# Kernel tuning notes

Hardware: AMD Instinct MI355X
Metric: run time of the kernel (lower is better)

## Reference

```python
import jax, jax.numpy as jnp
import numpy as np

GCN_DEPTH = 2
PROP_ALPHA = 0.05
TANH_ALPHA = 3.0
SUBGRAPH = 20
SCALE_SET = (1.0, 0.8, 0.6, 0.5)
LAYERS = 3


def _tconv(x, W, b, stride):
    # x: (B,C,N,L), W: (O,I,1,k) -> VALID temporal conv along L
    y = jax.lax.conv_general_dilated(x, W, (1, stride), 'VALID',
                                     dimension_numbers=('NCHW', 'OIHW', 'NCHW'))
    return y + b[None, :, None, None]


def _build_adj(feat_scale, emb1, emb2, W1, b1, W2, b2, sfac):
    # dynamic graph: time-pooled scale features + static node embeddings
    feat = feat_scale.mean(axis=3).transpose(0, 2, 1)            # (B,N,C)
    n1 = jnp.tanh(TANH_ALPHA * sfac * (feat @ W1 + b1 + emb1))   # (B,N,D)
    n2 = jnp.tanh(TANH_ALPHA * sfac * (feat @ W2 + b2 + emb2))
    a = jnp.einsum('bnd,bmd->bnm', n1, n2) - jnp.einsum('bnd,bmd->bnm', n2, n1)
    adj = jax.nn.relu(jnp.tanh(TANH_ALPHA * a))                  # (B,N,N)
    kth = jax.lax.top_k(adj, SUBGRAPH)[0][..., -1:]              # per-row k-th value
    return adj * (adj >= kth).astype(adj.dtype)


def _mixprop(x, adj, W, b):
    # x: (B,C,N,L), adj: (B,N,N); gcn_depth-step alpha-mixed diffusion
    N = x.shape[2]
    A = adj + jnp.eye(N, dtype=adj.dtype)
    A = A / A.sum(axis=2, keepdims=True)
    h = x
    out = [h]
    for _ in range(GCN_DEPTH):
        h = PROP_ALPHA * x + (1.0 - PROP_ALPHA) * jnp.einsum('bcvl,bvw->bcwl', h, A)
        out.append(h)
    ho = jnp.concatenate(out, axis=1)                            # (B,(gdep+1)C,N,L)
    return jnp.einsum('bcnl,co->bonl', ho, W) + b[None, :, None, None]


def _forward(x, Ws, bs, scW0, scW1, scW2, scb, emb1, emb2,
             lin1W, lin1b, lin2W, lin2b, gW, gb,
             svW0, svW1, svW2, svb, s0W, s0b,
             gfW1, gfW2, e1W, e1b, e2W, e2b):
    # multi-scale block: 1x1 start conv then strided temporal convs
    h = jnp.einsum('bcnl,oc->bonl', x, Ws) + bs[None, :, None, None]
    scW = [scW0, scW1, scW2]
    scales = []
    for i in range(LAYERS):
        h = _tconv(h, scW[i], scb[i], 1 if i == 0 else 2)
        scales.append(h)
    # per-scale dynamic adjacency
    adjs = [_build_adj(scales[i], emb1, emb2, lin1W[i], lin1b[i],
                       lin2W[i], lin2b[i], SCALE_SET[i]) for i in range(LAYERS)]
    # scale0 head over raw input (dropout is identity in eval mode)
    out0 = jnp.einsum('bcnl,ocl->bon', x, s0W)[..., None] + s0b[None, :, None, None]
    outs = [out0]
    svW = [svW0, svW1, svW2]
    for i in range(LAYERS):
        g = (_mixprop(scales[i], adjs[i], gW[i, 0], gb[i, 0])
             + _mixprop(scales[i], adjs[i].transpose(0, 2, 1), gW[i, 1], gb[i, 1]))
        outs.append(jnp.einsum('bcnl,ocl->bon', g, svW[i])[..., None]
                    + svb[i][None, :, None, None])
    cat = jnp.concatenate(outs, axis=1)          # (B,(L+1)*Cs,N,1)
    stk = jnp.stack(outs, axis=1)                # (B,L+1,Cs,N,1)
    # SE-style gated fusion over scales
    se = cat.mean(axis=2)[..., 0]                # (B,(L+1)*Cs)
    se = jax.nn.sigmoid(jax.nn.relu(se @ gfW1) @ gfW2)   # (B,L+1)
    fused = (stk * se[:, :, None, None, None]).mean(axis=1)  # (B,Cs,N,1)
    y = jax.nn.relu(fused)
    y = jax.nn.relu(jnp.einsum('bcnl,oc->bonl', y, e1W) + e1b[None, :, None, None])
    y = jnp.einsum('bcnl,oc->bonl', y, e2W) + e2b[None, :, None, None]
    return y, jnp.stack(adjs)


def setup_inputs() -> dict:
    key = jax.random.key(0)
    ks = jax.random.split(key, 27)
    B, N, S, D = 4, 600, 168, 40
    Cc, Cs, Ce, Od = 32, 16, 128, 12
    L = [162, 79, 39]
    K = [7, 6, 3]
    r = lambda k, sh, s=0.1: jax.random.normal(k, sh, jnp.float32) * s
    return {
        'x': jax.random.normal(ks[0], (B, 1, N, S), jnp.float32),
        'Ws': r(ks[1], (Cc, 1)), 'bs': r(ks[2], (Cc,)),
        'scW0': r(ks[3], (Cc, Cc, 1, K[0])), 'scW1': r(ks[4], (Cc, Cc, 1, K[1])),
        'scW2': r(ks[5], (Cc, Cc, 1, K[2])), 'scb': r(ks[6], (3, Cc)),
        'emb1': r(ks[7], (N, D), 1.0), 'emb2': r(ks[8], (N, D), 1.0),
        'lin1W': r(ks[9], (3, Cc, D)), 'lin1b': r(ks[10], (3, D)),
        'lin2W': r(ks[11], (3, Cc, D)), 'lin2b': r(ks[12], (3, D)),
        'gW': r(ks[13], (3, 2, 3 * Cc, Cc)), 'gb': r(ks[14], (3, 2, Cc)),
        'svW0': r(ks[15], (Cs, Cc, L[0])), 'svW1': r(ks[16], (Cs, Cc, L[1])),
        'svW2': r(ks[17], (Cs, Cc, L[2])), 'svb': r(ks[18], (3, Cs)),
        's0W': r(ks[19], (Cs, 1, S)), 's0b': r(ks[20], (Cs,)),
        'gfW1': r(ks[21], (4 * Cs, 4)), 'gfW2': r(ks[22], (4, 4)),
        'e1W': r(ks[23], (Ce, Cs)), 'e1b': r(ks[24], (Ce,)),
        'e2W': r(ks[25], (Od, Ce)), 'e2b': r(ks[26], (Od,)),
    }


def reference(x, Ws, bs, scW0, scW1, scW2, scb, emb1, emb2,
              lin1W, lin1b, lin2W, lin2b, gW, gb,
              svW0, svW1, svW2, svb, s0W, s0b,
              gfW1, gfW2, e1W, e1b, e2W, e2b):
    return _forward(x, Ws, bs, scW0, scW1, scW2, scb, emb1, emb2,
                    lin1W, lin1b, lin2W, lin2b, gW, gb,
                    svW0, svW1, svW2, svb, s0W, s0b,
                    gfW1, gfW2, e1W, e1b, e2W, e2b)
```

## Files before the change

### kernel.cpp

```cpp
#include <hip/hip_runtime.h>
#include <math.h>


#define DW_WEFF 0
#define DW_CC   1536
#define FB      3264
#define OW_CSV  (FB+0)
#define OW_CBIG (FB+48)
#define OW_VBIG (FB+304)
#define OW_U    (FB+43312)
#define OW_T    (FB+760112)
#define OW_FEAT (FB+1374512)
#define OW_N1   (FB+1604912)
#define OW_N2   (FB+1892912)
#define OW_IRA  (FB+2180912)
#define OW_IRB  (FB+2188112)
#define OW_U1A  (FB+2195312)
#define OW_U2A  (FB+2310512)
#define OW_U1B  (FB+2425712)
#define OW_U2B  (FB+2540912)
#define OW_U3A  (FB+2656112)
#define OW_U3B  (FB+2771312)
#define OW_O    (FB+2886512)
#define OW_SE   (FB+3040112)

__device__ const int UOFF_[3] = {0, 414720, 616960};

__device__ __forceinline__ float tanh_eigen(float x)
{
  const float CL = 7.99881172180175781f;
  float xc = fminf(fmaxf(x, -CL), CL);
  float x2 = __fmul_rn(xc, xc);
  float p = fmaf(x2, -2.76076847742355e-16f, 2.00018790482477e-13f);
  p = fmaf(x2, p, -8.60467152213735e-11f);
  p = fmaf(x2, p, 5.12229709037114e-08f);
  p = fmaf(x2, p, 1.48572235717979e-05f);
  p = fmaf(x2, p, 6.37261928875436e-04f);
  p = fmaf(x2, p, 4.89352455891786e-03f);
  p = __fmul_rn(xc, p);
  float q = fmaf(x2, 1.19825839466702e-06f, 1.18534705686654e-04f);
  q = fmaf(x2, q, 2.26843463243900e-03f);
  q = fmaf(x2, q, 4.89352518554385e-03f);
  float r = __fdiv_rn(p, q);
  return fabsf(x) < 0.0004f ? x : r;
}

__global__ __launch_bounds__(256) void k_pre_wc(const float* Ws, const float* bs,
    const float* scW0, const float* scW1, const float* scW2, const float* scb,
    const float* svW0, const float* svW1, const float* svW2,
    const float* gb, const float* svb, double* wd, float* ws)
{
  if (blockIdx.x < 48) {
    int blk = blockIdx.x;
    int i = blk/16, o = blk%16;
    const float* svW = (i==0)?svW0:((i==1)?svW1:svW2);
    int L = (i==0)?162:((i==1)?79:39);
    int tid = threadIdx.x;
    __shared__ double red[256];
    double s = 0;
    for (int idx = tid; idx < 32*L; idx += 256) {
      int o2 = idx / L, l = idx - o2*L;
      s += (double)svW[(o*32+o2)*L + l] * ((double)gb[(i*2+0)*32+o2] + (double)gb[(i*2+1)*32+o2]);
    }
    red[tid] = s; __syncthreads();
    for (int st = 128; st; st >>= 1) { if (tid < st) red[tid] += red[tid+st]; __syncthreads(); }
    if (tid == 0) ws[OW_CSV + blk] = (float)(red[0] + (double)svb[i*16+o]);
    return;
  }
  __shared__ double w0[32][7], c0[32], w1[32][12], c1[32];
  int t = threadIdx.x;
  for (int e = t; e < 32*7; e += 256) {
    int c = e/7, p = e%7; double s = 0;
    for (int ci = 0; ci < 32; ci++) s += (double)scW0[(c*32+ci)*7+p] * (double)Ws[ci];
    w0[c][p] = s;
  }
  for (int e = t; e < 32; e += 256) {
    double s = 0;
    for (int ci = 0; ci < 32; ci++) { double a = 0; for (int p = 0; p < 7; p++) a += (double)scW0[(e*32+ci)*7+p]; s += a*(double)bs[ci]; }
    c0[e] = s + (double)scb[e];
  }
  __syncthreads();
  for (int e = t; e < 32*12; e += 256) {
    int c = e/12, m = e%12; double s = 0;
    for (int k1 = 0; k1 < 6; k1++) { int k0 = m - k1; if (k0 < 0 || k0 > 6) continue;
      for (int ci = 0; ci < 32; ci++) s += (double)scW1[(c*32+ci)*6+k1] * w0[ci][k0]; }
    w1[c][m] = s;
  }
  for (int e = t; e < 32; e += 256) {
    double s = 0;
    for (int ci = 0; ci < 32; ci++) { double a = 0; for (int k1 = 0; k1 < 6; k1++) a += (double)scW1[(e*32+ci)*6+k1]; s += a*c0[ci]; }
    c1[e] = s + (double)scb[32+e];
  }
  __syncthreads();
  for (int e = t; e < 32*16; e += 256) {
    int c = e/16, p = e%16; double s = 0;
    for (int k2 = 0; k2 < 3; k2++) { int m = p - 2*k2; if (m < 0 || m > 11) continue;
      for (int ci = 0; ci < 32; ci++) s += (double)scW2[(c*32+ci)*3+k2] * w1[ci][m]; }
    wd[DW_WEFF + (2*32+c)*16 + p] = s;
  }
  for (int e = t; e < 32; e += 256) {
    double s = 0;
    for (int ci = 0; ci < 32; ci++) { double a = 0; for (int k2 = 0; k2 < 3; k2++) a += (double)scW2[(e*32+ci)*3+k2]; s += a*c1[ci]; }
    wd[DW_CC + 64 + e] = s + (double)scb[64+e];
  }
  for (int e = t; e < 32*7;  e += 256) wd[DW_WEFF + (e/7)*16  + e%7 ] = w0[e/7][e%7];
  for (int e = t; e < 32*12; e += 256) wd[DW_WEFF + (32 + e/12)*16 + e%12] = w1[e/12][e%12];
  for (int e = t; e < 32; e += 256) { wd[DW_CC+e] = c0[e]; wd[DW_CC+32+e] = c1[e]; }
}

__global__ void k_pre_u(const float* svW0, const float* svW1, const float* svW2,
                        const float* gW, float* ws)
{
  int blk = blockIdx.x;
  int i, L, base; const float* svW;
  if (blk < 1620)      { i=0; L=162; svW=svW0; base=0; }
  else if (blk < 2410) { i=1; L=79;  svW=svW1; base=1620; }
  else                 { i=2; L=39;  svW=svW2; base=2410; }
  int e = (blk-base)*256 + threadIdx.x;
  int total = 5*16*32*L;
  if (e >= total) return;
  int l = e % L, c = (e/L) % 32, o = (e/(L*32)) % 16, g = e/(L*32*16);
  const float* gW0 = gW + (i*2+0)*96*32;
  const float* gW1 = gW + (i*2+1)*96*32;
  float s = 0.f;
  for (int o2 = 0; o2 < 32; o2++) {
    float w;
    if (g == 0) w = gW0[c*32+o2] + gW1[c*32+o2]
                  + 0.05f*(gW0[(32+c)*32+o2] + gW0[(64+c)*32+o2] + gW1[(32+c)*32+o2] + gW1[(64+c)*32+o2]);
    else if (g == 1) w = gW0[(32+c)*32+o2];
    else if (g == 2) w = gW0[(64+c)*32+o2];
    else if (g == 3) w = gW1[(32+c)*32+o2];
    else             w = gW1[(64+c)*32+o2];
    s += svW[(o*32+o2)*L + l] * w;
  }
  ws[OW_U + UOFF_[i] + ((g*16+o)*32 + c)*L + l] = s;
}

__global__ __launch_bounds__(256) void k_pre_v(const float* s0W, const float* s0b, double* wd, float* ws)
{
  int jj = blockIdx.x;
  int tid = threadIdx.x;
  if (jj >= 240) {
    int o = jj - 240;
    if (tid < 168) ws[OW_VBIG + jj*168 + tid] = s0W[o*168 + tid];
    if (tid == 0)  ws[OW_CBIG + jj] = s0b[o];
    return;
  }
  int i = jj/80, g = (jj%80)/16, o = jj%16;
  int st = (i==0)?1:((i==1)?2:4), tp = (i==0)?7:((i==1)?12:16), L = (i==0)?162:((i==1)?79:39);
  const float* Ui = ws + OW_U + UOFF_[i] + ((g*16+o)*32)*L;
  __shared__ float uls[32*162];
  __shared__ double weff_s[32*16];
  __shared__ double cc_s[32];
  __shared__ double red[256];
  int NL = 32*L;
  for (int e = tid; e < NL; e += 256) uls[e] = Ui[e];
  for (int e = tid; e < 32*16; e += 256) weff_s[e] = wd[DW_WEFF + (i*32)*16 + e];
  if (tid < 32) cc_s[tid] = wd[DW_CC + i*32 + tid];
  __syncthreads();
  double s = 0;
  for (int e = tid; e < NL; e += 256) s += (double)uls[e] * cc_s[e / L];
  red[tid] = s; __syncthreads();
  for (int stp = 128; stp; stp >>= 1) { if (tid < stp) red[tid] += red[tid+stp]; __syncthreads(); }
  if (tid == 0) ws[OW_CBIG + jj] = (float)red[0];
  if (tid < 168) {
    int u = tid;
    int lo_ = u - tp + 1;
    int lmin = lo_ > 0 ? (lo_ + st - 1)/st : 0;
    int lmax = u/st; if (lmax > L-1) lmax = L-1;
    double v = 0.0;
    for (int c = 0; c < 32; c++) {
      const float* uc = uls + c*L;
      const double* wc = weff_s + c*16;
      for (int l = lmin; l <= lmax; l++)
        v += (double)uc[l] * wc[u - st*l];
    }
    ws[OW_VBIG + jj*168 + u] = (float)v;
  }
}

__global__ __launch_bounds__(256) void k_fg(const float* x, double* wd, float* ws)
{
  int t = threadIdx.x;
  if (blockIdx.x >= 300) {
    __shared__ float xs[16][168];
    int r0 = (blockIdx.x - 300)*16;
    for (int e = t; e < 16*168; e += 256) { int r = e/168, u = e%168; xs[r][u] = x[(r0+r)*168 + u]; }
    __syncthreads();
    int jj = t;
    const float* V = ws + OW_VBIG + jj*168;
    double a[16];
    #pragma unroll
    for (int r = 0; r < 16; r++) a[r] = 0;
    for (int u = 0; u < 168; u++) {
      float wv = V[u];
      #pragma unroll
      for (int r = 0; r < 16; r++) a[r] += (double)wv * (double)xs[r][u];
    }
    double cb = (double)ws[OW_CBIG + jj];
    for (int r = 0; r < 16; r++)
      ws[OW_T + (r0+r)*256 + jj] = (float)(a[r] + cb);
    return;
  }
  int blk = blockIdx.x;
  int b = blk / 75, n0 = (blk % 75) * 8;
  __shared__ float xsf[8][168];
  __shared__ double xbar[8][35];
  for (int e = t; e < 8*168; e += 256) xsf[e/168][e%168] = x[(b*600 + n0 + e/168)*168 + e%168];
  __syncthreads();
  for (int e = t; e < 8*35; e += 256) {
    int nn = e/35, slot = e%35;
    int i = slot < 7 ? 0 : (slot < 19 ? 1 : 2);
    int p = slot - (i==0?0:(i==1?7:19));
    int st = (i==0)?1:((i==1)?2:4), L = (i==0)?162:((i==1)?79:39);
    double s = 0;
    for (int l = 0; l < L; l++) s += (double)xsf[nn][st*l+p];
    xbar[nn][slot] = s / (double)L;
  }
  __syncthreads();
  int nn = t >> 5, c = t & 31;
  for (int i = 0; i < 3; i++) {
    int off = (i==0)?0:((i==1)?7:19), tp = (i==0)?7:((i==1)?12:16);
    double f = wd[DW_CC + i*32 + c];
    for (int p = 0; p < tp; p++) f += wd[DW_WEFF + (i*32+c)*16 + p] * xbar[nn][off+p];
    ws[OW_FEAT + ((i*4+b)*600 + n0+nn)*32 + c] = (float)f;
  }
}

__global__ __launch_bounds__(256) void k_nodes(const float* lin1W, const float* lin1b,
                                               const float* lin2W, const float* lin2b,
                                               const float* emb1, const float* emb2, float* ws)
{
  int blk = blockIdx.x;
  int nt = blk % 38, b = (blk/38) % 4, i = blk/152;
  int n0 = nt*16;
  __shared__ float W1[1280], W2[1280], b1[40], b2[40], sf[16][33];
  int t = threadIdx.x;
  for (int e = t; e < 1280; e += 256) { W1[e] = lin1W[i*1280 + e]; W2[e] = lin2W[i*1280 + e]; }
  if (t < 40) { b1[t] = lin1b[i*40 + t]; b2[t] = lin2b[i*40 + t]; }
  for (int e = t; e < 16*32; e += 256) {
    int nn = e >> 5, c = e & 31; int n = n0 + nn;
    sf[nn][c] = (n < 600) ? ws[OW_FEAT + ((i*4+b)*600 + n)*32 + c] : 0.f;
  }
  __syncthreads();
  const float TSF[3] = {3.0f, 2.4f, 1.8f};
  for (int item = t; item < 16*80; item += 256) {
    int nn = item / 80, rr = item % 80;
    int n = n0 + nn; if (n >= 600) continue;
    int which = rr/40, d = rr%40;
    const float* W  = which ? W2 : W1;
    const float* bv = which ? b2 : b1;
    const float* em = which ? emb2 : emb1;
    float pre = 0.f;
    #pragma unroll
    for (int c = 0; c < 32; c++) pre = fmaf(sf[nn][c], W[c*40+d], pre);
    float p2 = __fadd_rn(pre, bv[d]);
    float p3 = __fadd_rn(p2, em[n*40+d]);
    float arg = __fmul_rn(TSF[i], p3);
    ws[(which ? OW_N2 : OW_N1) + ((i*4+b)*600 + n)*40 + d] = tanh_eigen(arg);
  }
}

__device__ __forceinline__ float4 adj_ld(const float* n1, const float* n2, int e, int w0)
{
  int mat = e >= 320; int idx = e - 320*mat;
  int jj = idx/10, q = idx - 10*jj;
  int w = w0 + jj;
  if (w < 600) return *(const float4*)((mat ? n2 : n1) + w*40 + 4*q);
  float4 z; z.x = z.y = z.z = z.w = 0.f; return z;
}

__global__ __launch_bounds__(256) void k_adj(float* adj_out, float* ws)
{
  int blk = blockIdx.x;
  int tile = blk % 75, b = (blk/75) % 4, i = blk/300;
  int row0 = tile*8;
  const float* n1 = ws + OW_N1 + (i*4+b)*24000;
  const float* n2 = ws + OW_N2 + (i*4+b)*24000;
  __shared__ float c1s[32][44], c2s[32][44];
  __shared__ float svals[8][604];
  int t = threadIdx.x;
  int rc = t & 7, jc = t >> 3;
  float am1[40], am2[40];
  {
    const float4* m1p = (const float4*)(n1 + (row0 + rc)*40);
    const float4* m2p = (const float4*)(n2 + (row0 + rc)*40);
    #pragma unroll
    for (int q = 0; q < 10; q++) {
      float4 v1 = m1p[q], v2 = m2p[q];
      am1[4*q]=v1.x; am1[4*q+1]=v1.y; am1[4*q+2]=v1.z; am1[4*q+3]=v1.w;
      am2[4*q]=v2.x; am2[4*q+1]=v2.y; am2[4*q+2]=v2.z; am2[4*q+3]=v2.w;
    }
  }
  float4 s0 = adj_ld(n1, n2, t, 0);
  float4 s1 = adj_ld(n1, n2, t + 256, 0);
  float4 s2; if (t < 128) s2 = adj_ld(n1, n2, t + 512, 0);
  for (int k = 0; k < 19; k++) {
    int w0 = 32*k;
    __syncthreads();
    {
      int e = t;       { int mat=e>=320, idx=e-320*mat, jj=idx/10, q=idx-10*jj, w=w0+jj;
                         if (w<600) *(float4*)(&(mat?c2s:c1s)[jj][4*q]) = s0; }
      e = t + 256;     { int mat=e>=320, idx=e-320*mat, jj=idx/10, q=idx-10*jj, w=w0+jj;
                         if (w<600) *(float4*)(&(mat?c2s:c1s)[jj][4*q]) = s1; }
      if (t < 128) { e = t + 512; int mat=e>=320, idx=e-320*mat, jj=idx/10, q=idx-10*jj, w=w0+jj;
                         if (w<600) *(float4*)(&(mat?c2s:c1s)[jj][4*q]) = s2; }
    }
    __syncthreads();
    if (k < 18) {
      int w0n = w0 + 32;
      s0 = adj_ld(n1, n2, t, w0n);
      s1 = adj_ld(n1, n2, t + 256, w0n);
      if (t < 128) s2 = adj_ld(n1, n2, t + 512, w0n);
    }
    int w = w0 + jc;
    if (w < 600) {
      const float4* c2p = (const float4*)c2s[jc];
      const float4* c1p = (const float4*)c1s[jc];
      float d1 = 0.f, d2 = 0.f;
      #pragma unroll
      for (int q = 0; q < 10; q++) {
        float4 v = c2p[q];
        d1 = fmaf(am1[4*q], v.x, d1); d1 = fmaf(am1[4*q+1], v.y, d1);
        d1 = fmaf(am1[4*q+2], v.z, d1); d1 = fmaf(am1[4*q+3], v.w, d1);
      }
      #pragma unroll
      for (int q = 0; q < 10; q++) {
        float4 v = c1p[q];
        d2 = fmaf(am2[4*q], v.x, d2); d2 = fmaf(am2[4*q+1], v.y, d2);
        d2 = fmaf(am2[4*q+2], v.z, d2); d2 = fmaf(am2[4*q+3], v.w, d2);
      }
      float af = __fsub_rn(d1, d2);
      float tv = __fmul_rn(3.0f, af);
      float v = tanh_eigen(tv);
      svals[rc][w] = v > 0.f ? v : 0.f;
    }
  }
  __syncthreads();
  int r = t >> 5, j = t & 31;
  float vv[19];
  #pragma unroll
  for (int k = 0; k < 19; k++) {
    int w = j + 32*k;
    vv[k] = (w < 600) ? svals[r][w] : 0.f;
  }
  float rm = 0.f;
  #pragma unroll
  for (int k = 0; k < 19; k++) rm = fmaxf(rm, vv[k]);
  #pragma unroll
  for (int s = 16; s; s >>= 1) rm = fmaxf(rm, __shfl_xor(rm, s, 32));
  const float VP = tanh_eigen(8.0f);
  unsigned int vpb = __float_as_uint(VP);
  int cntp = 0;
  #pragma unroll
  for (int k = 0; k < 19; k++) { int w = j + 32*k; if (w < 600 && __float_as_uint(vv[k]) >= vpb) cntp++; }
  #pragma unroll
  for (int s = 16; s; s >>= 1) cntp += __shfl_xor(cntp, s, 32);
  unsigned int lo, hi;
  unsigned int mb1 = __float_as_uint(rm) + 1u;
  if (cntp >= 20) { lo = vpb; hi = mb1; }
  else            { lo = 0u;  hi = vpb < mb1 ? vpb : mb1; }
  while (hi - lo > 1u) {
    unsigned int mid = lo + ((hi - lo) >> 1);
    int cnt = 0;
    #pragma unroll
    for (int k = 0; k < 19; k++) {
      int w = j + 32*k;
      if (w < 600 && __float_as_uint(vv[k]) >= mid) cnt++;
    }
    #pragma unroll
    for (int s = 16; s; s >>= 1) cnt += __shfl_xor(cnt, s, 32);
    if (cnt >= 20) lo = mid; else hi = mid;
  }
  unsigned int kb = lo;
  float* arow = adj_out + (i*4+b)*360000 + (row0+r)*600;
  float rsum = 0.f;
  #pragma unroll
  for (int k = 0; k < 19; k++) {
    int w = j + 32*k;
    if (w < 600) {
      float v = (__float_as_uint(vv[k]) >= kb) ? vv[k] : 0.f;
      arow[w] = v;
      rsum += v;
    }
  }
  #pragma unroll
  for (int s = 16; s; s >>= 1) rsum += __shfl_xor(rsum, s, 32);
  if (j == 0) ws[OW_IRA + (i*4+b)*600 + row0 + r] = 1.f/(1.f + rsum);
}

__global__ __launch_bounds__(256) void k_invrb(const float* adj, float* ws)
{
  int blk = blockIdx.x;
  int ib = blk / 10, wt = blk % 10;
  int tid = threadIdx.x;
  int wl = tid & 63, vg = tid >> 6;
  int w = wt*64 + wl;
  const float* A = adj + ib*360000;
  float s = 0.f;
  if (w < 600) {
    for (int v = vg*150; v < vg*150 + 150; v++) s += A[v*600 + w];
  }
  __shared__ float red[4][64];
  red[vg][wl] = s;
  __syncthreads();
  if (vg == 0 && w < 600) {
    float tot = ((red[0][wl] + red[1][wl]) + red[2][wl]) + red[3][wl];
    ws[OW_IRB + ib*600 + w] = 1.f/(1.f + tot);
  }
}

__global__ __launch_bounds__(256) void k_prop1(const float* adj, float* ws)
{
  int blk = blockIdx.x;
  int wt = blk % 19;
  int d  = (blk / 19) & 1;
  int ib = blk / 38;
  int i = ib >> 2, b = ib & 3;
  int w0 = wt * 32;
  const float* A   = adj + ib*360000;
  const float* irx = ws + (d ? OW_IRB : OW_IRA) + ib*600;
  const float* Tb  = ws + OW_T + (b*600)*256 + i*80 + 16 + d*32;
  __shared__ float As[4][32][36];
  __shared__ float Zs[4][32][36];
  __shared__ float red[3][64][17];
  int tid = threadIdx.x;
  int wv = tid >> 6, ln = tid & 63;
  int wq = ln >> 3, oq = ln & 7;
  float acc[4][4];
  #pragma unroll
  for (int a1 = 0; a1 < 4; a1++)
    #pragma unroll
    for (int a2 = 0; a2 < 4; a2++) acc[a1][a2] = 0.f;
  int vbeg = wv*160, vend = vbeg + 160 < 600 ? vbeg + 160 : 600;
  for (int v0 = vbeg; v0 < vend; v0 += 32) {
    if (d == 0) {
      #pragma unroll
      for (int q = 0; q < 4; q++) {
        int m = q*64 + ln, rr = m >> 3, c4 = (m & 7)*4;
        int v = v0 + rr;
        float4 av; av.x = av.y = av.z = av.w = 0.f;
        if (v < 600) {
          int wb = w0 + c4;
          if (wb + 3 < 600) av = *(const float4*)(A + v*600 + wb);
          else {
            if (wb+0 < 600) av.x = A[v*600 + wb+0];
            if (wb+1 < 600) av.y = A[v*600 + wb+1];
            if (wb+2 < 600) av.z = A[v*600 + wb+2];
            if (wb+3 < 600) av.w = A[v*600 + wb+3];
          }
        }
        *(float4*)(&As[wv][rr][c4]) = av;
      }
    } else {
      #pragma unroll
      for (int q = 0; q < 4; q++) {
        int m = q*64 + ln, rr = m >> 3, c4 = (m & 7)*4;
        int w = w0 + rr;
        float4 av; av.x = av.y = av.z = av.w = 0.f;
        if (w < 600) {
          if (v0 + c4 + 3 < 600) av = *(const float4*)(A + w*600 + v0 + c4);
          else {
            if (v0+c4+0 < 600) av.x = A[w*600 + v0+c4+0];
            if (v0+c4+1 < 600) av.y = A[w*600 + v0+c4+1];
            if (v0+c4+2 < 600) av.z = A[w*600 + v0+c4+2];
            if (v0+c4+3 < 600) av.w = A[w*600 + v0+c4+3];
          }
        }
        As[wv][c4+0][rr] = av.x; As[wv][c4+1][rr] = av.y;
        As[wv][c4+2][rr] = av.z; As[wv][c4+3][rr] = av.w;
      }
    }
    #pragma unroll
    for (int q = 0; q < 4; q++) {
      int m = q*64 + ln, rr = m >> 3, c4 = (m & 7)*4;
      int v = v0 + rr;
      float4 zv; zv.x = zv.y = zv.z = zv.w = 0.f;
      if (v < 600) {
        float ir = irx[v];
        float4 tv = *(const float4*)(Tb + v*256 + c4);
        zv.x = ir*tv.x; zv.y = ir*tv.y; zv.z = ir*tv.z; zv.w = ir*tv.w;
      }
      *(float4*)(&Zs[wv][rr][c4]) = zv;
    }
    __builtin_amdgcn_s_waitcnt(0);
    for (int vl = 0; vl < 32; vl++) {
      float4 a4 = *(const float4*)(&As[wv][vl][wq*4]);
      float4 z4 = *(const float4*)(&Zs[wv][vl][oq*4]);
      acc[0][0] = fmaf(a4.x, z4.x, acc[0][0]); acc[0][1] = fmaf(a4.x, z4.y, acc[0][1]);
      acc[0][2] = fmaf(a4.x, z4.z, acc[0][2]); acc[0][3] = fmaf(a4.x, z4.w, acc[0][3]);
      acc[1][0] = fmaf(a4.y, z4.x, acc[1][0]); acc[1][1] = fmaf(a4.y, z4.y, acc[1][1]);
      acc[1][2] = fmaf(a4.y, z4.z, acc[1][2]); acc[1][3] = fmaf(a4.y, z4.w, acc[1][3]);
      acc[2][0] = fmaf(a4.z, z4.x, acc[2][0]); acc[2][1] = fmaf(a4.z, z4.y, acc[2][1]);
      acc[2][2] = fmaf(a4.z, z4.z, acc[2][2]); acc[2][3] = fmaf(a4.z, z4.w, acc[2][3]);
      acc[3][0] = fmaf(a4.w, z4.x, acc[3][0]); acc[3][1] = fmaf(a4.w, z4.y, acc[3][1]);
      acc[3][2] = fmaf(a4.w, z4.z, acc[3][2]); acc[3][3] = fmaf(a4.w, z4.w, acc[3][3]);
    }
  }
  if (wv > 0) {
    #pragma unroll
    for (int kw = 0; kw < 4; kw++)
      #pragma unroll
      for (int ko = 0; ko < 4; ko++) red[wv-1][ln][kw*4+ko] = acc[kw][ko];
  }
  __syncthreads();
  if (wv == 0) {
    #pragma unroll
    for (int kw = 0; kw < 4; kw++) {
      int w = w0 + wq*4 + kw;
      if (w >= 600) continue;
      float irw = irx[w];
      #pragma unroll
      for (int ko = 0; ko < 4; ko++) {
        int oz = oq*4 + ko;
        float sum = acc[kw][ko] + red[0][ln][kw*4+ko] + red[1][ln][kw*4+ko] + red[2][ln][kw*4+ko];
        sum += irw * Tb[w*256 + oz];
        float* dst = ws + (d==0 ? (oz < 16 ? OW_U1A : OW_U2A) : (oz < 16 ? OW_U1B : OW_U2B));
        dst[(ib*600 + w)*16 + (oz & 15)] = sum;
      }
    }
  }
}

__global__ __launch_bounds__(256) void k_prop2(const float* adj, float* ws)
{
  int blk = blockIdx.x;
  int wt = blk % 19;
  int d  = (blk / 19) & 1;
  int ib = blk / 38;
  int w0 = wt * 32;
  const float* A   = adj + ib*360000;
  const float* irx = ws + (d ? OW_IRB : OW_IRA) + ib*600;
  const float* u2x = ws + (d ? OW_U2B : OW_U2A) + ib*9600;
  __shared__ float As[4][32][36];
  __shared__ float Zs[4][32][20];
  __shared__ float red[3][64][9];
  int tid = threadIdx.x;
  int wv = tid >> 6, ln = tid & 63;
  int wq = ln >> 3, oq = ln & 7;
  float acc[4][2];
  #pragma unroll
  for (int a1 = 0; a1 < 4; a1++) { acc[a1][0] = 0.f; acc[a1][1] = 0.f; }
  int vbeg = wv*160, vend = vbeg + 160 < 600 ? vbeg + 160 : 600;
  for (int v0 = vbeg; v0 < vend; v0 += 32) {
    if (d == 0) {
      #pragma unroll
      for (int q = 0; q < 4; q++) {
        int m = q*64 + ln, rr = m >> 3, c4 = (m & 7)*4;
        int v = v0 + rr;
        float4 av; av.x = av.y = av.z = av.w = 0.f;
        if (v < 600) {
          int wb = w0 + c4;
          if (wb + 3 < 600) av = *(const float4*)(A + v*600 + wb);
          else {
            if (wb+0 < 600) av.x = A[v*600 + wb+0];
            if (wb+1 < 600) av.y = A[v*600 + wb+1];
            if (wb+2 < 600) av.z = A[v*600 + wb+2];
            if (wb+3 < 600) av.w = A[v*600 + wb+3];
          }
        }
        *(float4*)(&As[wv][rr][c4]) = av;
      }
    } else {
      #pragma unroll
      for (int q = 0; q < 4; q++) {
        int m = q*64 + ln, rr = m >> 3, c4 = (m & 7)*4;
        int w = w0 + rr;
        float4 av; av.x = av.y = av.z = av.w = 0.f;
        if (w < 600) {
          if (v0 + c4 + 3 < 600) av = *(const float4*)(A + w*600 + v0 + c4);
          else {
            if (v0+c4+0 < 600) av.x = A[w*600 + v0+c4+0];
            if (v0+c4+1 < 600) av.y = A[w*600 + v0+c4+1];
            if (v0+c4+2 < 600) av.z = A[w*600 + v0+c4+2];
            if (v0+c4+3 < 600) av.w = A[w*600 + v0+c4+3];
          }
        }
        As[wv][c4+0][rr] = av.x; As[wv][c4+1][rr] = av.y;
        As[wv][c4+2][rr] = av.z; As[wv][c4+3][rr] = av.w;
      }
    }
    #pragma unroll
    for (int q = 0; q < 2; q++) {
      int m = q*64 + ln, rr = m >> 2, c4 = (m & 3)*4;
      int v = v0 + rr;
      float4 zv; zv.x = zv.y = zv.z = zv.w = 0.f;
      if (v < 600) {
        float ir = irx[v];
        float4 uv = *(const float4*)(u2x + v*16 + c4);
        zv.x = ir*uv.x; zv.y = ir*uv.y; zv.z = ir*uv.z; zv.w = ir*uv.w;
      }
      *(float4*)(&Zs[wv][rr][c4]) = zv;
    }
    __builtin_amdgcn_s_waitcnt(0);
    for (int vl = 0; vl < 32; vl++) {
      float4 a4 = *(const float4*)(&As[wv][vl][wq*4]);
      float2 z2 = *(const float2*)(&Zs[wv][vl][oq*2]);
      acc[0][0] = fmaf(a4.x, z2.x, acc[0][0]); acc[0][1] = fmaf(a4.x, z2.y, acc[0][1]);
      acc[1][0] = fmaf(a4.y, z2.x, acc[1][0]); acc[1][1] = fmaf(a4.y, z2.y, acc[1][1]);
      acc[2][0] = fmaf(a4.z, z2.x, acc[2][0]); acc[2][1] = fmaf(a4.z, z2.y, acc[2][1]);
      acc[3][0] = fmaf(a4.w, z2.x, acc[3][0]); acc[3][1] = fmaf(a4.w, z2.y, acc[3][1]);
    }
  }
  if (wv > 0) {
    #pragma unroll
    for (int kw = 0; kw < 4; kw++) {
      red[wv-1][ln][kw*2+0] = acc[kw][0];
      red[wv-1][ln][kw*2+1] = acc[kw][1];
    }
  }
  __syncthreads();
  if (wv == 0) {
    float* dst = ws + (d==0 ? OW_U3A : OW_U3B);
    #pragma unroll
    for (int kw = 0; kw < 4; kw++) {
      int w = w0 + wq*4 + kw;
      if (w >= 600) continue;
      float irw = irx[w];
      #pragma unroll
      for (int ko = 0; ko < 2; ko++) {
        int oz = oq*2 + ko;
        float sum = acc[kw][ko] + red[0][ln][kw*2+ko] + red[1][ln][kw*2+ko] + red[2][ln][kw*2+ko];
        sum += irw * u2x[w*16 + oz];
        dst[(ib*600 + w)*16 + oz] = sum;
      }
    }
  }
}

__global__ void k_outs(float* ws)
{
  int e = blockIdx.x*256 + threadIdx.x;
  if (e >= 153600) return;
  int n = e % 600, o = (e/600) % 16, b = (e/9600) % 4, s = e/38400;
  float val;
  if (s == 0) {
    val = ws[OW_T + (b*600+n)*256 + 240 + o];
  } else {
    int i = s - 1;
    int idx = ((i*4+b)*600 + n)*16 + o;
    float t0 = ws[OW_T + (b*600+n)*256 + i*80 + o];
    val = t0 + 0.95f  * (ws[OW_U1A+idx] + ws[OW_U1B+idx])
             + 0.0475f* (ws[OW_U2A+idx] + ws[OW_U2B+idx])
             + 0.9025f* (ws[OW_U3A+idx] + ws[OW_U3B+idx])
             + ws[OW_CSV + i*16 + o];
  }
  ws[OW_O + ((s*4+b)*16 + o)*600 + n] = val;
}

__global__ void k_se(const float* gfW1, const float* gfW2, float* ws)
{
  __shared__ float sv[4][64], hb[4][4];
  int t = threadIdx.x, b = t >> 6, k = t & 63;
  const float* Op = ws + OW_O + (((k>>4)*4 + b)*16 + (k & 15))*600;
  float s = 0.f;
  for (int n = 0; n < 600; n++) s += Op[n];
  sv[b][k] = s * (1.f/600.f);
  __syncthreads();
  if (t < 16) {
    int bb = t >> 2, j = t & 3;
    float h = 0.f;
    for (int kk = 0; kk < 64; kk++) h += sv[bb][kk]*gfW1[kk*4+j];
    hb[bb][j] = h > 0.f ? h : 0.f;
  }
  __syncthreads();
  if (t < 16) {
    int bb = t >> 2, ii = t & 3;
    float g = 0.f;
    for (int j = 0; j < 4; j++) g += hb[bb][j]*gfW2[j*4+ii];
    ws[OW_SE + bb*4 + ii] = 1.f/(1.f + expf(-g));
  }
}

__global__ __launch_bounds__(128) void k_head(const float* e1W, const float* e1b,
                                              const float* e2W, const float* e2b,
                                              float* ws, float* dout)
{
  int blk = blockIdx.x, b = blk/600, n = blk%600;
  __shared__ float y0[16], y1[128];
  int t = threadIdx.x;
  if (t < 16) {
    float f = 0.f;
    for (int s = 0; s < 4; s++) f += ws[OW_SE + b*4 + s] * ws[OW_O + ((s*4+b)*16 + t)*600 + n];
    f *= 0.25f;
    y0[t] = f > 0.f ? f : 0.f;
  }
  __syncthreads();
  {
    float h = e1b[t];
    for (int o = 0; o < 16; o++) h += e1W[t*16+o]*y0[o];
    y1[t] = h > 0.f ? h : 0.f;
  }
  __syncthreads();
  if (t < 96) {
    int o = t >> 3, part = t & 7;
    float v = 0.f;
    #pragma unroll
    for (int e = 0; e < 16; e++) v = fmaf(e2W[o*128 + part*16 + e], y1[part*16 + e], v);
    #pragma unroll
    for (int s = 4; s; s >>= 1) v += __shfl_down(v, s, 8);
    if (part == 0) dout[b*7200 + o*600 + n] = e2b[o] + v;
  }
}

extern "C" void kernel_launch(void* const* d_in, const int* in_sizes, int n_in,
                              void* d_out, int out_size, void* d_ws, size_t ws_size,
                              hipStream_t stream)
{
  const float* x    = (const float*)d_in[0];
  const float* Ws   = (const float*)d_in[1];
  const float* bs   = (const float*)d_in[2];
  const float* scW0 = (const float*)d_in[3];
  const float* scW1 = (const float*)d_in[4];
  const float* scW2 = (const float*)d_in[5];
  const float* scb  = (const float*)d_in[6];
  const float* emb1 = (const float*)d_in[7];
  const float* emb2 = (const float*)d_in[8];
  const float* lin1W= (const float*)d_in[9];
  const float* lin1b= (const float*)d_in[10];
  const float* lin2W= (const float*)d_in[11];
  const float* lin2b= (const float*)d_in[12];
  const float* gW   = (const float*)d_in[13];
  const float* gb   = (const float*)d_in[14];
  const float* svW0 = (const float*)d_in[15];
  const float* svW1 = (const float*)d_in[16];
  const float* svW2 = (const float*)d_in[17];
  const float* svb  = (const float*)d_in[18];
  const float* s0W  = (const float*)d_in[19];
  const float* s0b  = (const float*)d_in[20];
  const float* gfW1 = (const float*)d_in[21];
  const float* gfW2 = (const float*)d_in[22];
  const float* e1W  = (const float*)d_in[23];
  const float* e1b  = (const float*)d_in[24];
  const float* e2W  = (const float*)d_in[25];
  const float* e2b  = (const float*)d_in[26];
  float* out = (float*)d_out;
  float* ws  = (float*)d_ws;
  double* wd = (double*)d_ws;
  float* adj_out = out + 28800;

  k_pre_wc<<<49, 256, 0, stream>>>(Ws, bs, scW0, scW1, scW2, scb,
                                   svW0, svW1, svW2, gb, svb, wd, ws);
  k_pre_u<<<2800, 256, 0, stream>>>(svW0, svW1, svW2, gW, ws);
  k_pre_v<<<256, 256, 0, stream>>>(s0W, s0b, wd, ws);
  k_fg<<<450, 256, 0, stream>>>(x, wd, ws);
  k_nodes<<<456, 256, 0, stream>>>(lin1W, lin1b, lin2W, lin2b, emb1, emb2, ws);
  k_adj<<<900, 256, 0, stream>>>(adj_out, ws);
  k_invrb<<<120, 256, 0, stream>>>(adj_out, ws);
  k_prop1<<<456, 256, 0, stream>>>(adj_out, ws);
  k_prop2<<<456, 256, 0, stream>>>(adj_out, ws);
  k_outs<<<600, 256, 0, stream>>>(ws);
  k_se<<<1, 256, 0, stream>>>(gfW1, gfW2, ws);
  k_head<<<2400, 128, 0, stream>>>(e1W, e1b, e2W, e2b, ws, out);
}
```

Before: 266.5 us.

## Merge weight-precompute kernels and read adjacency node vectors directly from global

Folds the k_pre_u blocks into k_pre_wc as extra blocks of a single launch, removing one kernel launch and its inter-kernel gap. In k_adj, the double-buffered shared-memory staging of n1/n2 column tiles and its two per-iteration barriers are replaced by direct float4 loads from global memory, relying on cache for reuse. This cuts barriers and shared-memory traffic but may add global/L2 load pressure, since the 8 threads sharing a column each fetch it themselves.

```diff
diff --git a/kernel.cpp b/kernel.cpp
--- a/kernel.cpp
+++ b/kernel.cpp
@@ -45,26 +45,52 @@
   return fabsf(x) < 0.0004f ? x : r;
 }
 
-__global__ __launch_bounds__(256) void k_pre_wc(const float* Ws, const float* bs,
+__global__ __launch_bounds__(256) void k_pre_wcu(const float* Ws, const float* bs,
     const float* scW0, const float* scW1, const float* scW2, const float* scb,
     const float* svW0, const float* svW1, const float* svW2,
-    const float* gb, const float* svb, double* wd, float* ws)
-{
+    const float* gb, const float* svb, const float* gW, double* wd, float* ws)
+{
+  if (blockIdx.x >= 49) {
+    int blk = blockIdx.x - 49;
+    int i, L, base; const float* svW;
+    if (blk < 1620)      { i=0; L=162; svW=svW0; base=0; }
+    else if (blk < 2410) { i=1; L=79;  svW=svW1; base=1620; }
+    else                 { i=2; L=39;  svW=svW2; base=2410; }
+    int e = (blk-base)*256 + threadIdx.x;
+    int total = 5*16*32*L;
+    if (e >= total) return;
+    int l = e % L, c = (e/L) % 32, o = (e/(L*32)) % 16, g = e/(L*32*16);
+    const float* gW0 = gW + (i*2+0)*96*32;
+    const float* gW1 = gW + (i*2+1)*96*32;
+    float s = 0.f;
+    for (int o2 = 0; o2 < 32; o2++) {
+      float w;
+      if (g == 0) w = gW0[c*32+o2] + gW1[c*32+o2]
+                    + 0.05f*(gW0[(32+c)*32+o2] + gW0[(64+c)*32+o2] + gW1[(32+c)*32+o2] + gW1[(64+c)*32+o2]);
+      else if (g == 1) w = gW0[(32+c)*32+o2];
+      else if (g == 2) w = gW0[(64+c)*32+o2];
+      else if (g == 3) w = gW1[(32+c)*32+o2];
+      else             w = gW1[(64+c)*32+o2];
+      s += svW[(o*32+o2)*L + l] * w;
+    }
+    ws[OW_U + UOFF_[i] + ((g*16+o)*32 + c)*L + l] = s;
+    return;
+  }
   if (blockIdx.x < 48) {
     int blk = blockIdx.x;
     int i = blk/16, o = blk%16;
     const float* svW = (i==0)?svW0:((i==1)?svW1:svW2);
     int L = (i==0)?162:((i==1)?79:39);
     int tid = threadIdx.x;
-    __shared__ double red[256];
+    __shared__ double redc[256];
     double s = 0;
     for (int idx = tid; idx < 32*L; idx += 256) {
       int o2 = idx / L, l = idx - o2*L;
       s += (double)svW[(o*32+o2)*L + l] * ((double)gb[(i*2+0)*32+o2] + (double)gb[(i*2+1)*32+o2]);
     }
-    red[tid] = s; __syncthreads();
-    for (int st = 128; st; st >>= 1) { if (tid < st) red[tid] += red[tid+st]; __syncthreads(); }
-    if (tid == 0) ws[OW_CSV + blk] = (float)(red[0] + (double)svb[i*16+o]);
+    redc[tid] = s; __syncthreads();
+    for (int st = 128; st; st >>= 1) { if (tid < st) redc[tid] += redc[tid+st]; __syncthreads(); }
+    if (tid == 0) ws[OW_CSV + blk] = (float)(redc[0] + (double)svb[i*16+o]);
     return;
   }
   __shared__ double w0[32][7], c0[32], w1[32][12], c1[32];
@@ -106,34 +132,6 @@
   for (int e = t; e < 32*7;  e += 256) wd[DW_WEFF + (e/7)*16  + e%7 ] = w0[e/7][e%7];
   for (int e = t; e < 32*12; e += 256) wd[DW_WEFF + (32 + e/12)*16 + e%12] = w1[e/12][e%12];
   for (int e = t; e < 32; e += 256) { wd[DW_CC+e] = c0[e]; wd[DW_CC+32+e] = c1[e]; }
-}
-
-__global__ void k_pre_u(const float* svW0, const float* svW1, const float* svW2,
-                        const float* gW, float* ws)
-{
-  int blk = blockIdx.x;
-  int i, L, base; const float* svW;
-  if (blk < 1620)      { i=0; L=162; svW=svW0; base=0; }
-  else if (blk < 2410) { i=1; L=79;  svW=svW1; base=1620; }
-  else                 { i=2; L=39;  svW=svW2; base=2410; }
-  int e = (blk-base)*256 + threadIdx.x;
-  int total = 5*16*32*L;
-  if (e >= total) return;
-  int l = e % L, c = (e/L) % 32, o = (e/(L*32)) % 16, g = e/(L*32*16);
-  const float* gW0 = gW + (i*2+0)*96*32;
-  const float* gW1 = gW + (i*2+1)*96*32;
-  float s = 0.f;
-  for (int o2 = 0; o2 < 32; o2++) {
-    float w;
-    if (g == 0) w = gW0[c*32+o2] + gW1[c*32+o2]
-                  + 0.05f*(gW0[(32+c)*32+o2] + gW0[(64+c)*32+o2] + gW1[(32+c)*32+o2] + gW1[(64+c)*32+o2]);
-    else if (g == 1) w = gW0[(32+c)*32+o2];
-    else if (g == 2) w = gW0[(64+c)*32+o2];
-    else if (g == 3) w = gW1[(32+c)*32+o2];
-    else             w = gW1[(64+c)*32+o2];
-    s += svW[(o*32+o2)*L + l] * w;
-  }
-  ws[OW_U + UOFF_[i] + ((g*16+o)*32 + c)*L + l] = s;
 }
 
 __global__ __launch_bounds__(256) void k_pre_v(const float* s0W, const float* s0b, double* wd, float* ws)
@@ -261,15 +259,6 @@
   }
 }
 
-__device__ __forceinline__ float4 adj_ld(const float* n1, const float* n2, int e, int w0)
-{
-  int mat = e >= 320; int idx = e - 320*mat;
-  int jj = idx/10, q = idx - 10*jj;
-  int w = w0 + jj;
-  if (w < 600) return *(const float4*)((mat ? n2 : n1) + w*40 + 4*q);
-  float4 z; z.x = z.y = z.z = z.w = 0.f; return z;
-}
-
 __global__ __launch_bounds__(256) void k_adj(float* adj_out, float* ws)
 {
   int blk = blockIdx.x;
@@ -277,7 +266,6 @@
   int row0 = tile*8;
   const float* n1 = ws + OW_N1 + (i*4+b)*24000;
   const float* n2 = ws + OW_N2 + (i*4+b)*24000;
-  __shared__ float c1s[32][44], c2s[32][44];
   __shared__ float svals[8][604];
   int t = threadIdx.x;
   int rc = t & 7, jc = t >> 3;
@@ -292,31 +280,11 @@
       am2[4*q]=v2.x; am2[4*q+1]=v2.y; am2[4*q+2]=v2.z; am2[4*q+3]=v2.w;
     }
   }
-  float4 s0 = adj_ld(n1, n2, t, 0);
-  float4 s1 = adj_ld(n1, n2, t + 256, 0);
-  float4 s2; if (t < 128) s2 = adj_ld(n1, n2, t + 512, 0);
   for (int k = 0; k < 19; k++) {
-    int w0 = 32*k;
-    __syncthreads();
-    {
-      int e = t;       { int mat=e>=320, idx=e-320*mat, jj=idx/10, q=idx-10*jj, w=w0+jj;
-                         if (w<600) *(float4*)(&(mat?c2s:c1s)[jj][4*q]) = s0; }
-      e = t + 256;     { int mat=e>=320, idx=e-320*mat, jj=idx/10, q=idx-10*jj, w=w0+jj;
-                         if (w<600) *(float4*)(&(mat?c2s:c1s)[jj][4*q]) = s1; }
-      if (t < 128) { e = t + 512; int mat=e>=320, idx=e-320*mat, jj=idx/10, q=idx-10*jj, w=w0+jj;
-                         if (w<600) *(float4*)(&(mat?c2s:c1s)[jj][4*q]) = s2; }
-    }
-    __syncthreads();
-    if (k < 18) {
-      int w0n = w0 + 32;
-      s0 = adj_ld(n1, n2, t, w0n);
-      s1 = adj_ld(n1, n2, t + 256, w0n);
-      if (t < 128) s2 = adj_ld(n1, n2, t + 512, w0n);
-    }
-    int w = w0 + jc;
+    int w = jc + 32*k;
     if (w < 600) {
-      const float4* c2p = (const float4*)c2s[jc];
-      const float4* c1p = (const float4*)c1s[jc];
+      const float4* c2p = (const float4*)(n2 + w*40);
+      const float4* c1p = (const float4*)(n1 + w*40);
       float d1 = 0.f, d2 = 0.f;
       #pragma unroll
       for (int q = 0; q < 10; q++) {
@@ -739,9 +707,8 @@
   double* wd = (double*)d_ws;
   float* adj_out = out + 28800;
 
-  k_pre_wc<<<49, 256, 0, stream>>>(Ws, bs, scW0, scW1, scW2, scb,
-                                   svW0, svW1, svW2, gb, svb, wd, ws);
-  k_pre_u<<<2800, 256, 0, stream>>>(svW0, svW1, svW2, gW, ws);
+  k_pre_wcu<<<2849, 256, 0, stream>>>(Ws, bs, scW0, scW1, scW2, scb,
+                                      svW0, svW1, svW2, gb, svb, gW, wd, ws);
   k_pre_v<<<256, 256, 0, stream>>>(s0W, s0b, wd, ws);
   k_fg<<<450, 256, 0, stream>>>(x, wd, ws);
   k_nodes<<<456, 256, 0, stream>>>(lin1W, lin1b, lin2W, lin2b, emb1, emb2, ws);
```

Result: faster. 257.0 us (-3.6%).

## Reassociate weight-folding precompute to contract gW with effective conv weights first

Applied to the files above, without the earlier changes.

Replaces the large per-element U precompute (svW times gW over all L positions, 2800 blocks) with a small 15-block kernel that first contracts gW with the effective temporal-conv weights and bias terms into P and Q. k_pre_v then combines svW directly with P from shared memory, and the bias term is computed from row sums of svW times Q. This removes a large intermediate buffer write and read and much of the redundant arithmetic. It also guards the adjacency inner loop on jc<32, which may change which threads do the dot products.

```diff
diff --git a/kernel.cpp b/kernel.cpp
--- a/kernel.cpp
+++ b/kernel.cpp
@@ -4,11 +4,11 @@
 
 #define DW_WEFF 0
 #define DW_CC   1536
-#define FB      3264
+#define DW_P    1632
+#define FB      18624
 #define OW_CSV  (FB+0)
 #define OW_CBIG (FB+48)
 #define OW_VBIG (FB+304)
-#define OW_U    (FB+43312)
 #define OW_T    (FB+760112)
 #define OW_FEAT (FB+1374512)
 #define OW_N1   (FB+1604912)
@@ -23,8 +23,6 @@
 #define OW_U3B  (FB+2771312)
 #define OW_O    (FB+2886512)
 #define OW_SE   (FB+3040112)
-
-__device__ const int UOFF_[3] = {0, 414720, 616960};
 
 __device__ __forceinline__ float tanh_eigen(float x)
 {
@@ -45,6 +43,18 @@
   return fabsf(x) < 0.0004f ? x : r;
 }
 
+__device__ __forceinline__ float wg_val(const float* gW, int i, int g, int c, int o2)
+{
+  const float* gW0 = gW + (i*2+0)*96*32;
+  const float* gW1 = gW + (i*2+1)*96*32;
+  if (g == 0) return gW0[c*32+o2] + gW1[c*32+o2]
+                + 0.05f*(gW0[(32+c)*32+o2] + gW0[(64+c)*32+o2] + gW1[(32+c)*32+o2] + gW1[(64+c)*32+o2]);
+  else if (g == 1) return gW0[(32+c)*32+o2];
+  else if (g == 2) return gW0[(64+c)*32+o2];
+  else if (g == 3) return gW1[(32+c)*32+o2];
+  return gW1[(64+c)*32+o2];
+}
+
 __global__ __launch_bounds__(256) void k_pre_wc(const float* Ws, const float* bs,
     const float* scW0, const float* scW1, const float* scW2, const float* scb,
     const float* svW0, const float* svW1, const float* svW2,
@@ -108,35 +118,51 @@
   for (int e = t; e < 32; e += 256) { wd[DW_CC+e] = c0[e]; wd[DW_CC+32+e] = c1[e]; }
 }
 
-__global__ void k_pre_u(const float* svW0, const float* svW1, const float* svW2,
-                        const float* gW, float* ws)
+__global__ __launch_bounds__(256) void k_pre_p(const float* svW0, const float* svW1, const float* svW2,
+                                               const float* gW, double* wd, float* ws)
 {
   int blk = blockIdx.x;
-  int i, L, base; const float* svW;
-  if (blk < 1620)      { i=0; L=162; svW=svW0; base=0; }
-  else if (blk < 2410) { i=1; L=79;  svW=svW1; base=1620; }
-  else                 { i=2; L=39;  svW=svW2; base=2410; }
-  int e = (blk-base)*256 + threadIdx.x;
-  int total = 5*16*32*L;
-  if (e >= total) return;
-  int l = e % L, c = (e/L) % 32, o = (e/(L*32)) % 16, g = e/(L*32*16);
-  const float* gW0 = gW + (i*2+0)*96*32;
-  const float* gW1 = gW + (i*2+1)*96*32;
-  float s = 0.f;
-  for (int o2 = 0; o2 < 32; o2++) {
-    float w;
-    if (g == 0) w = gW0[c*32+o2] + gW1[c*32+o2]
-                  + 0.05f*(gW0[(32+c)*32+o2] + gW0[(64+c)*32+o2] + gW1[(32+c)*32+o2] + gW1[(64+c)*32+o2]);
-    else if (g == 1) w = gW0[(32+c)*32+o2];
-    else if (g == 2) w = gW0[(64+c)*32+o2];
-    else if (g == 3) w = gW1[(32+c)*32+o2];
-    else             w = gW1[(64+c)*32+o2];
-    s += svW[(o*32+o2)*L + l] * w;
-  }
-  ws[OW_U + UOFF_[i] + ((g*16+o)*32 + c)*L + l] = s;
-}
-
-__global__ __launch_bounds__(256) void k_pre_v(const float* s0W, const float* s0b, double* wd, float* ws)
+  int i = blk/5, g = blk%5;
+  const float* svW = (i==0)?svW0:((i==1)?svW1:svW2);
+  int L = (i==0)?162:((i==1)?79:39);
+  int tid = threadIdx.x;
+  for (int e = tid; e < 512; e += 256) {
+    int o2 = e >> 4, p = e & 15;
+    double s = 0;
+    for (int c = 0; c < 32; c++)
+      s += (double)wg_val(gW,i,g,c,o2) * wd[DW_WEFF + (i*32+c)*16 + p];
+    wd[DW_P + ((i*5+g)*32 + o2)*16 + p] = s;
+  }
+  __shared__ double Qs[32];
+  __shared__ double cbred[16][17];
+  if (tid < 32) {
+    double s = 0;
+    for (int c = 0; c < 32; c++)
+      s += (double)wg_val(gW,i,g,c,tid) * wd[DW_CC + i*32 + c];
+    Qs[tid] = s;
+  }
+  __syncthreads();
+  {
+    int o = tid >> 4, part = tid & 15;
+    double s = 0;
+    for (int o2 = part*2; o2 < part*2+2; o2++) {
+      double sl = 0;
+      const float* sv = svW + (o*32+o2)*L;
+      for (int l = 0; l < L; l++) sl += (double)sv[l];
+      s += sl * Qs[o2];
+    }
+    cbred[o][part] = s;
+  }
+  __syncthreads();
+  if (tid < 16) {
+    double s = 0;
+    for (int p = 0; p < 16; p++) s += cbred[tid][p];
+    ws[OW_CBIG + (i*80 + g*16 + tid)] = (float)s;
+  }
+}
+
+__global__ __launch_bounds__(256) void k_pre_v(const float* svW0, const float* svW1, const float* svW2,
+                                               const float* s0W, const float* s0b, double* wd, float* ws)
 {
   int jj = blockIdx.x;
   int tid = threadIdx.x;
@@ -148,32 +174,28 @@
   }
   int i = jj/80, g = (jj%80)/16, o = jj%16;
   int st = (i==0)?1:((i==1)?2:4), tp = (i==0)?7:((i==1)?12:16), L = (i==0)?162:((i==1)?79:39);
-  const float* Ui = ws + OW_U + UOFF_[i] + ((g*16+o)*32)*L;
-  __shared__ float uls[32*162];
-  __shared__ double weff_s[32*16];
-  __shared__ double cc_s[32];
-  __shared__ double red[256];
+  const float* svW = (i==0)?svW0:((i==1)?svW1:svW2);
+  const float* svo = svW + o*32*L;
+  __shared__ float svlds[32*162];
+  __shared__ double Pl[32][16];
   int NL = 32*L;
-  for (int e = tid; e < NL; e += 256) uls[e] = Ui[e];
-  for (int e = tid; e < 32*16; e += 256) weff_s[e] = wd[DW_WEFF + (i*32)*16 + e];
-  if (tid < 32) cc_s[tid] = wd[DW_CC + i*32 + tid];
-  __syncthreads();
-  double s = 0;
-  for (int e = tid; e < NL; e += 256) s += (double)uls[e] * cc_s[e / L];
-  red[tid] = s; __syncthreads();
-  for (int stp = 128; stp; stp >>= 1) { if (tid < stp) red[tid] += red[tid+stp]; __syncthreads(); }
-  if (tid == 0) ws[OW_CBIG + jj] = (float)red[0];
+  for (int e = tid; e < NL; e += 256) svlds[e] = svo[e];
+  for (int e = tid; e < 512; e += 256) {
+    int o2 = e >> 4, p = e & 15;
+    Pl[o2][p] = wd[DW_P + ((i*5+g)*32 + o2)*16 + p];
+  }
+  __syncthreads();
   if (tid < 168) {
     int u = tid;
     int lo_ = u - tp + 1;
     int lmin = lo_ > 0 ? (lo_ + st - 1)/st : 0;
     int lmax = u/st; if (lmax > L-1) lmax = L-1;
     double v = 0.0;
-    for (int c = 0; c < 32; c++) {
-      const float* uc = uls + c*L;
-      const double* wc = weff_s + c*16;
+    for (int o2 = 0; o2 < 32; o2++) {
+      const float* sv = svlds + o2*L;
+      const double* Pp = Pl[o2];
       for (int l = lmin; l <= lmax; l++)
-        v += (double)uc[l] * wc[u - st*l];
+        v += (double)sv[l] * Pp[u - st*l];
     }
     ws[OW_VBIG + jj*168 + u] = (float)v;
   }
@@ -313,27 +335,30 @@
       s1 = adj_ld(n1, n2, t + 256, w0n);
       if (t < 128) s2 = adj_ld(n1, n2, t + 512, w0n);
     }
-    int w = w0 + jc;
-    if (w < 600) {
-      const float4* c2p = (const float4*)c2s[jc];
-      const float4* c1p = (const float4*)c1s[jc];
-      float d1 = 0.f, d2 = 0.f;
-      #pragma unroll
-      for (int q = 0; q < 10; q++) {
-        float4 v = c2p[q];
-        d1 = fmaf(am1[4*q], v.x, d1); d1 = fmaf(am1[4*q+1], v.y, d1);
-        d1 = fmaf(am1[4*q+2], v.z, d1); d1 = fmaf(am1[4*q+3], v.w, d1);
-      }
-      #pragma unroll
-      for (int q = 0; q < 10; q++) {
-        float4 v = c1p[q];
-        d2 = fmaf(am2[4*q], v.x, d2); d2 = fmaf(am2[4*q+1], v.y, d2);
-        d2 = fmaf(am2[4*q+2], v.z, d2); d2 = fmaf(am2[4*q+3], v.w, d2);
-      }
-      float af = __fsub_rn(d1, d2);
-      float tv = __fmul_rn(3.0f, af);
-      float v = tanh_eigen(tv);
-      svals[rc][w] = v > 0.f ? v : 0.f;
+    int jcl = jc & 31;
+    if (jc < 32) {
+      int w = w0 + jcl;
+      if (w < 600) {
+        const float4* c2p = (const float4*)c2s[jcl];
+        const float4* c1p = (const float4*)c1s[jcl];
+        float d1 = 0.f, d2 = 0.f;
+        #pragma unroll
+        for (int q = 0; q < 10; q++) {
+          float4 v = c2p[q];
+          d1 = fmaf(am1[4*q], v.x, d1); d1 = fmaf(am1[4*q+1], v.y, d1);
+          d1 = fmaf(am1[4*q+2], v.z, d1); d1 = fmaf(am1[4*q+3], v.w, d1);
+        }
+        #pragma unroll
+        for (int q = 0; q < 10; q++) {
+          float4 v = c1p[q];
+          d2 = fmaf(am2[4*q], v.x, d2); d2 = fmaf(am2[4*q+1], v.y, d2);
+          d2 = fmaf(am2[4*q+2], v.z, d2); d2 = fmaf(am2[4*q+3], v.w, d2);
+        }
+        float af = __fsub_rn(d1, d2);
+        float tv = __fmul_rn(3.0f, af);
+        float v = tanh_eigen(tv);
+        svals[rc][w] = v > 0.f ? v : 0.f;
+      }
     }
   }
   __syncthreads();
@@ -741,8 +766,8 @@
 
   k_pre_wc<<<49, 256, 0, stream>>>(Ws, bs, scW0, scW1, scW2, scb,
                                    svW0, svW1, svW2, gb, svb, wd, ws);
-  k_pre_u<<<2800, 256, 0, stream>>>(svW0, svW1, svW2, gW, ws);
-  k_pre_v<<<256, 256, 0, stream>>>(s0W, s0b, wd, ws);
+  k_pre_p<<<15, 256, 0, stream>>>(svW0, svW1, svW2, gW, wd, ws);
+  k_pre_v<<<256, 256, 0, stream>>>(svW0, svW1, svW2, s0W, s0b, wd, ws);
   k_fg<<<450, 256, 0, stream>>>(x, wd, ws);
   k_nodes<<<456, 256, 0, stream>>>(lin1W, lin1b, lin2W, lin2b, emb1, emb2, ws);
   k_adj<<<900, 256, 0, stream>>>(adj_out, ws);
```

Result: slower. 342.6 us (+28.5%).
